# Kernel tuning notes

Measured on AMD Instinct MI355X. Metric: run time of the kernel, lower is better.

Reference implementation:

```python
import jax, jax.numpy as jnp
import numpy as np

NEG_POS_RATIO = 3
BETA = 1.0
ALPHA = 2.0


def _smooth_ex_loss(pred, tgt):
    # a = beta / (1 - exp(-alpha)); c = a - beta - beta/alpha
    a = BETA / (1.0 - np.exp(-ALPHA))
    c = a - BETA - BETA / ALPHA
    diff = jnp.abs(pred - tgt)
    return jnp.where(diff < 1.0,
                     a * (diff + (jnp.exp(-ALPHA * diff) - 1.0) / ALPHA),
                     BETA * diff + c)


def setup_inputs() -> dict:
    key = jax.random.key(0)
    k1, k2, k3, k4 = jax.random.split(key, 4)
    B, P, C = 128, 8732, 21
    return {
        "confidence": jax.random.normal(k1, (B, P, C), dtype=jnp.float32),
        "predicted_locations": jax.random.normal(k2, (B, P, 4), dtype=jnp.float32),
        "labels": jax.random.randint(k3, (B, P), 0, C, dtype=jnp.int64),
        "gt_locations": jax.random.normal(k4, (B, P, 4), dtype=jnp.float32),
    }


def reference(confidence, predicted_locations, labels, gt_locations):
    # confidence: [B, P, C]; labels: [B, P]; locations: [B, P, 4]
    logp = jax.nn.log_softmax(confidence, axis=2)
    pos_mask = labels > 0

    # --- hard negative mining (no-grad in original) ---
    bg_loss = jax.lax.stop_gradient(-logp[:, :, 0])          # [B, P]
    num_pos = pos_mask.sum(axis=1, keepdims=True)             # [B, 1]
    num_neg = num_pos * NEG_POS_RATIO
    mined = jnp.where(pos_mask, -jnp.inf, bg_loss)
    idx = jnp.argsort(-mined, axis=1)                         # descending sort
    orders = jnp.argsort(idx, axis=1)                         # rank of each prior
    neg_mask = orders < num_neg
    mask = pos_mask | neg_mask                                # [B, P]

    # --- classification loss: sum of CE over mined priors ---
    per_elem_ce = -jnp.take_along_axis(logp, labels[..., None], axis=2)[..., 0]
    classification_loss = jnp.sum(jnp.where(mask, per_elem_ce, 0.0))

    # --- localization loss: smooth-ex loss over positive priors ---
    loc = _smooth_ex_loss(predicted_locations, gt_locations)  # [B, P, 4]
    smooth_sum = jnp.sum(jnp.where(pos_mask[..., None], loc, 0.0))

    n_pos_total = pos_mask.sum().astype(jnp.float32)
    return (smooth_sum / n_pos_total, classification_loss / n_pos_total)
```

## Files before the change

kernel.cpp:

```cpp
#include <hip/hip_runtime.h>
#include <cstdint>


#define B_ 128
#define P_ 8732
#define C_ 21
constexpr int TPB = 256;
constexpr int TILE = 256;
constexpr int TPBATCH = 35;
constexpr int TAILCNT = P_ - (TPBATCH - 1) * TILE;
constexpr int NTILES = B_ * TPBATCH;
constexpr int TPBLK = 4;
constexpr int GRID = NTILES / TPBLK;
constexpr int TILE_F = TILE * C_;
constexpr int NCHUNK = TILE_F * 4 / 1024;

typedef const __attribute__((address_space(1))) uint32_t* gas_u32p;
typedef __attribute__((address_space(3))) uint32_t* las_u32p;

__device__ __forceinline__ float waveSumF(float v) {
#pragma unroll
  for (int o = 32; o; o >>= 1) v += __shfl_down(v, o);
  return v;
}
__device__ __forceinline__ int waveSumI(int v) {
#pragma unroll
  for (int o = 32; o; o >>= 1) v += __shfl_down(v, o);
  return v;
}
__device__ __forceinline__ double waveSumD(double v) {
#pragma unroll
  for (int o = 32; o; o >>= 1) v += __shfl_down(v, o);
  return v;
}

__device__ __forceinline__ void stage_tile(const float* __restrict__ src,
                                           float* dst, const char* clampEnd,
                                           int wid, int lane) {
  const char* base = (const char*)src;
  for (int j = wid; j < NCHUNK; j += 4) {
    const char* s = base + j * 1024 + lane * 16;
    if (s > clampEnd) s = clampEnd;
    __builtin_amdgcn_global_load_lds((gas_u32p)s, (las_u32p)(dst + j * 256), 16, 0, 0);
  }
}

__global__ __launch_bounds__(TPB) void k_main(
    const float* __restrict__ conf, const float* __restrict__ pred,
    const int* __restrict__ labels, const float* __restrict__ gt,
    float2* __restrict__ part, float* __restrict__ ceneg, int* __restrict__ npos) {
  __shared__ __align__(16) float tile[2][TILE_F];
  const int tid = threadIdx.x;
  const int wid = tid >> 6, lane = tid & 63;
  const int tau0 = blockIdx.x * TPBLK;
  const int b_first = tau0 / TPBATCH;
  const char* clampEnd = (const char*)conf + (size_t)B_ * P_ * C_ * 4 - 16;
  const float4* pred4 = (const float4*)pred;
  const float4* gt4 = (const float4*)gt;

  {
    const int b = tau0 / TPBATCH, x = tau0 - b * TPBATCH;
    stage_tile(conf + ((size_t)b * P_ + x * TILE) * C_, tile[0], clampEnd, wid, lane);
  }
  int lab_r;
  float4 pr_r, gt_r;
  {
    const int b = tau0 / TPBATCH, x = tau0 - b * TPBATCH;
    size_t gp = (size_t)b * P_ + (size_t)x * TILE + tid;
    if (gp > (size_t)B_ * P_ - 1) gp = (size_t)B_ * P_ - 1;
    lab_r = labels[gp];
    pr_r = pred4[gp];
    gt_r = gt4[gp];
  }
  __syncthreads();

  float sm_acc = 0.f, cp_acc = 0.f, cn0 = 0.f, cn1 = 0.f;
  int np0 = 0, np1 = 0;

#pragma unroll
  for (int k = 0; k < TPBLK; ++k) {
    const int tau = tau0 + k;
    const int cur = k & 1;

    int lab_n = 0;
    float4 pr_n = make_float4(0, 0, 0, 0), gt_n = pr_n;
    if (k + 1 < TPBLK) {
      const int tn = tau + 1;
      const int bn = tn / TPBATCH, xn = tn - bn * TPBATCH;
      stage_tile(conf + ((size_t)bn * P_ + xn * TILE) * C_, tile[cur ^ 1], clampEnd, wid, lane);
      size_t gp = (size_t)bn * P_ + (size_t)xn * TILE + tid;
      if (gp > (size_t)B_ * P_ - 1) gp = (size_t)B_ * P_ - 1;
      lab_n = labels[gp];
      pr_n = pred4[gp];
      gt_n = gt4[gp];
    }

    const int b = tau / TPBATCH, x = tau - b * TPBATCH;
    const int cnt = (x == TPBATCH - 1) ? TAILCNT : TILE;
    if (tid < cnt) {
      const float* row = &tile[cur][tid * C_];
      float m = row[0];
#pragma unroll
      for (int c = 1; c < C_; ++c) m = fmaxf(m, row[c]);
      float s = 0.f;
#pragma unroll
      for (int c = 0; c < C_; ++c) s += __expf(row[c] - m);
      const float lse = m + __logf(s);
      const float ce = lse - row[lab_r];
      float ce_neg = 0.f;
      int np = 0;
      if (lab_r > 0) {
        np = 1;
        cp_acc += ce;
        const float A = 1.1565176427496657f;
        const float Cc = -0.3434823572503343f;
        float d;
        d = fabsf(pr_r.x - gt_r.x); sm_acc += (d < 1.f) ? A * (d + (__expf(-2.f * d) - 1.f) * 0.5f) : d + Cc;
        d = fabsf(pr_r.y - gt_r.y); sm_acc += (d < 1.f) ? A * (d + (__expf(-2.f * d) - 1.f) * 0.5f) : d + Cc;
        d = fabsf(pr_r.z - gt_r.z); sm_acc += (d < 1.f) ? A * (d + (__expf(-2.f * d) - 1.f) * 0.5f) : d + Cc;
        d = fabsf(pr_r.w - gt_r.w); sm_acc += (d < 1.f) ? A * (d + (__expf(-2.f * d) - 1.f) * 0.5f) : d + Cc;
      } else {
        ce_neg = ce;
      }
      if (b == b_first) { cn0 += ce_neg; np0 += np; }
      else             { cn1 += ce_neg; np1 += np; }
    }

    __syncthreads();
    lab_r = lab_n; pr_r = pr_n; gt_r = gt_n;
  }

  float sm = waveSumF(sm_acc), cp = waveSumF(cp_acc);
  float c0 = waveSumF(cn0), c1 = waveSumF(cn1);
  int n0 = waveSumI(np0), n1 = waveSumI(np1);
  float* red = tile[0];
  int* redi = (int*)red;
  if (lane == 0) {
    red[wid] = sm; red[4 + wid] = cp; red[8 + wid] = c0; red[12 + wid] = c1;
    redi[16 + wid] = n0; redi[20 + wid] = n1;
  }
  __syncthreads();
  if (tid == 0) {
    float SM = 0, CP = 0, C0 = 0, C1 = 0;
    int N0 = 0, N1 = 0;
#pragma unroll
    for (int w = 0; w < 4; ++w) {
      SM += red[w]; CP += red[4 + w]; C0 += red[8 + w]; C1 += red[12 + w];
      N0 += redi[16 + w]; N1 += redi[20 + w];
    }
    part[blockIdx.x] = make_float2(SM, CP);
    atomicAdd(&ceneg[b_first], C0);
    atomicAdd(&npos[b_first], N0);
    const int b_last = (tau0 + TPBLK - 1) / TPBATCH;
    if (b_last != b_first) {
      atomicAdd(&ceneg[b_last], C1);
      atomicAdd(&npos[b_last], N1);
    }
  }
}

__global__ __launch_bounds__(TPB) void k_decide(double* __restrict__ g,
                                                const float2* __restrict__ part,
                                                const float* __restrict__ ceneg,
                                                const int* __restrict__ npos,
                                                int* __restrict__ flags) {
  const int tid = threadIdx.x;
  const int wid = tid >> 6, lane = tid & 63;
  __shared__ double sd0[4], sd1[4], sd2[4];
  __shared__ int si[4];

  double sm = 0.0, cp = 0.0;
  for (int i = tid; i < GRID; i += TPB) {
    const float2 v = part[i];
    sm += (double)v.x;
    cp += (double)v.y;
  }
  sm = waveSumD(sm);
  cp = waveSumD(cp);
  if (lane == 0) { sd0[wid] = sm; sd1[wid] = cp; }
  __syncthreads();
  if (tid == 0) {
    g[0] = sd0[0] + sd0[1] + sd0[2] + sd0[3];
    g[1] = sd1[0] + sd1[1] + sd1[2] + sd1[3];
  }
  __syncthreads();

  double cn = 0.0;
  int n = 0;
  if (tid < B_) {
    const int np = npos[tid];
    const int need = 3 * np;
    const int nav = P_ - np;
    int fl = 0;
    if (need >= nav) cn = (double)ceneg[tid]; else fl = 1;
    flags[tid] = fl;
    n = np;
  }
  cn = waveSumD(cn);
  n = waveSumI(n);
  if (lane == 0) { sd2[wid] = cn; si[wid] = n; }
  __syncthreads();
  if (tid == 0) {
    g[2] = sd2[0] + sd2[1] + sd2[2] + sd2[3];
    g[3] = (double)(si[0] + si[1] + si[2] + si[3]);
  }
}

__device__ __forceinline__ unsigned keyCE(const float* __restrict__ conf,
                                          const int* __restrict__ labels,
                                          int b, int p, float& ce) {
  const float* row = conf + ((size_t)b * P_ + p) * C_;
  float m = row[0];
  for (int c = 1; c < C_; ++c) m = fmaxf(m, row[c]);
  float s = 0.f;
  for (int c = 0; c < C_; ++c) s += __expf(row[c] - m);
  const float lse = m + __logf(s);
  const int lab = labels[(size_t)b * P_ + p];
  ce = lse - row[lab];
  if (lab > 0) return 0u;
  unsigned u = __float_as_uint(lse - row[0]);
  u = (u & 0x80000000u) ? ~u : (u | 0x80000000u);
  return u ? u : 1u;
}

__global__ __launch_bounds__(TPB) void k_fallback(const float* __restrict__ conf,
                                                  const int* __restrict__ labels,
                                                  double* __restrict__ g,
                                                  const int* __restrict__ npos,
                                                  const int* __restrict__ flags) {
  const int b = blockIdx.x;
  if (!flags[b]) return;
  const int tid = threadIdx.x;
  const int need = 3 * npos[b];
  __shared__ int icnt[4];
  __shared__ float fsum[4];

  unsigned long long lo = 1, hi = 0xFFFFFFFFull, ans = 1;
  while (lo <= hi) {
    const unsigned long long mid = lo + ((hi - lo) >> 1);
    int c = 0;
    float dummy;
    for (int p = tid; p < P_; p += TPB)
      if ((unsigned long long)keyCE(conf, labels, b, p, dummy) >= mid) c++;
    c = waveSumI(c);
    if ((tid & 63) == 0) icnt[tid >> 6] = c;
    __syncthreads();
    const int tot = icnt[0] + icnt[1] + icnt[2] + icnt[3];
    if (tot >= need) { ans = mid; lo = mid + 1; } else { hi = mid - 1; }
    __syncthreads();
  }

  int cgt = 0;
  float sgt = 0.f;
  for (int p = tid; p < P_; p += TPB) {
    float ce;
    const unsigned long long k = keyCE(conf, labels, b, p, ce);
    if (k > ans) { cgt++; sgt += ce; }
  }
  cgt = waveSumI(cgt);
  sgt = waveSumF(sgt);
  if ((tid & 63) == 0) { icnt[tid >> 6] = cgt; fsum[tid >> 6] = sgt; }
  __syncthreads();
  if (tid == 0) {
    const int gtot = icnt[0] + icnt[1] + icnt[2] + icnt[3];
    double s = (double)(fsum[0] + fsum[1] + fsum[2] + fsum[3]);
    int r = need - gtot;
    int taken = 0;
    for (int p = 0; p < P_ && taken < r; ++p) {
      float ce;
      if (keyCE(conf, labels, b, p, ce) == ans) { s += ce; taken++; }
    }
    atomicAdd(&g[2], s);
  }
}

__global__ void k_final(const double* __restrict__ g, float* __restrict__ out) {
  out[0] = (float)(g[0] / g[3]);
  out[1] = (float)((g[1] + g[2]) / g[3]);
}

extern "C" void kernel_launch(void* const* d_in, const int* in_sizes, int n_in,
                              void* d_out, int out_size, void* d_ws, size_t ws_size,
                              hipStream_t stream) {
  const float* conf = (const float*)d_in[0];
  const float* pred = (const float*)d_in[1];
  const int* labels = (const int*)d_in[2];
  const float* gt = (const float*)d_in[3];
  float* out = (float*)d_out;

  double* g = (double*)d_ws;
  float* ceneg = (float*)(g + 8);
  int* npos = (int*)(ceneg + B_);
  int* flags = npos + B_;
  float2* part = (float2*)(flags + B_);
  const size_t zbytes = 8 * sizeof(double) + B_ * sizeof(float) + B_ * sizeof(int);
  hipMemsetAsync(d_ws, 0, zbytes, stream);

  hipLaunchKernelGGL(k_main, dim3(GRID), dim3(TPB), 0, stream,
                     conf, pred, labels, gt, part, ceneg, npos);
  hipLaunchKernelGGL(k_decide, dim3(1), dim3(TPB), 0, stream, g, part, ceneg, npos, flags);
  hipLaunchKernelGGL(k_fallback, dim3(B_), dim3(TPB), 0, stream, conf, labels, g, npos, flags);
  hipLaunchKernelGGL(k_final, dim3(1), dim3(1), 0, stream, g, out);
}
```

Baseline: 39.13 us.

## Merge decide, fallback and final kernels into one tail kernel; halve block size

Replaces the three post-processing kernels (decide, fallback, final) with a single one-block tail kernel that reduces the partials, runs the per-batch fallback selection serially when needed, and writes the output directly. This removes two kernel launches and their launch gaps. Separately, the main kernel moves to 128-thread blocks with 128-prior tiles, so it launches twice as many blocks, and staging now skips out-of-range chunks instead of clamping the address. The fallback path is now serialized across batches in one block, which would be very slow if any batch ever needs it.

Result: slower. 48.26 us (+23.3%).

```diff
diff --git a/kernel.cpp b/kernel.cpp
--- a/kernel.cpp
+++ b/kernel.cpp
@@ -5,15 +5,15 @@
 #define B_ 128
 #define P_ 8732
 #define C_ 21
-constexpr int TPB = 256;
-constexpr int TILE = 256;
-constexpr int TPBATCH = 35;
-constexpr int TAILCNT = P_ - (TPBATCH - 1) * TILE;
-constexpr int NTILES = B_ * TPBATCH;
+constexpr int TPB = 128;
+constexpr int TILE = 128;
+constexpr int TPROW = 69;
+constexpr int TAILCNT = P_ - (TPROW - 1) * TILE;
+constexpr int NTILES = B_ * TPROW;
 constexpr int TPBLK = 4;
 constexpr int GRID = NTILES / TPBLK;
 constexpr int TILE_F = TILE * C_;
-constexpr int NCHUNK = TILE_F * 4 / 1024;
+constexpr int NCHUNK = 11;
 
 typedef const __attribute__((address_space(1))) uint32_t* gas_u32p;
 typedef __attribute__((address_space(3))) uint32_t* las_u32p;
@@ -35,13 +35,14 @@
 }
 
 __device__ __forceinline__ void stage_tile(const float* __restrict__ src,
-                                           float* dst, const char* clampEnd,
+                                           float* dst, int tilebytes,
                                            int wid, int lane) {
   const char* base = (const char*)src;
-  for (int j = wid; j < NCHUNK; j += 4) {
-    const char* s = base + j * 1024 + lane * 16;
-    if (s > clampEnd) s = clampEnd;
-    __builtin_amdgcn_global_load_lds((gas_u32p)s, (las_u32p)(dst + j * 256), 16, 0, 0);
+  for (int j = wid; j < NCHUNK; j += 2) {
+    const int off = (j << 10) + (lane << 4);
+    if (off < tilebytes)
+      __builtin_amdgcn_global_load_lds((gas_u32p)(base + off),
+                                       (las_u32p)(dst + (j << 8)), 16, 0, 0);
   }
 }
 
@@ -53,19 +54,19 @@
   const int tid = threadIdx.x;
   const int wid = tid >> 6, lane = tid & 63;
   const int tau0 = blockIdx.x * TPBLK;
-  const int b_first = tau0 / TPBATCH;
-  const char* clampEnd = (const char*)conf + (size_t)B_ * P_ * C_ * 4 - 16;
+  const int b_first = tau0 / TPROW;
   const float4* pred4 = (const float4*)pred;
   const float4* gt4 = (const float4*)gt;
 
   {
-    const int b = tau0 / TPBATCH, x = tau0 - b * TPBATCH;
-    stage_tile(conf + ((size_t)b * P_ + x * TILE) * C_, tile[0], clampEnd, wid, lane);
+    const int b = tau0 / TPROW, x = tau0 - b * TPROW;
+    const int tb = ((x == TPROW - 1) ? TAILCNT : TILE) * (C_ * 4);
+    stage_tile(conf + ((size_t)b * P_ + (size_t)x * TILE) * C_, tile[0], tb, wid, lane);
   }
   int lab_r;
   float4 pr_r, gt_r;
   {
-    const int b = tau0 / TPBATCH, x = tau0 - b * TPBATCH;
+    const int b = tau0 / TPROW, x = tau0 - b * TPROW;
     size_t gp = (size_t)b * P_ + (size_t)x * TILE + tid;
     if (gp > (size_t)B_ * P_ - 1) gp = (size_t)B_ * P_ - 1;
     lab_r = labels[gp];
@@ -86,8 +87,9 @@
     float4 pr_n = make_float4(0, 0, 0, 0), gt_n = pr_n;
     if (k + 1 < TPBLK) {
       const int tn = tau + 1;
-      const int bn = tn / TPBATCH, xn = tn - bn * TPBATCH;
-      stage_tile(conf + ((size_t)bn * P_ + xn * TILE) * C_, tile[cur ^ 1], clampEnd, wid, lane);
+      const int bn = tn / TPROW, xn = tn - bn * TPROW;
+      const int tb = ((xn == TPROW - 1) ? TAILCNT : TILE) * (C_ * 4);
+      stage_tile(conf + ((size_t)bn * P_ + (size_t)xn * TILE) * C_, tile[cur ^ 1], tb, wid, lane);
       size_t gp = (size_t)bn * P_ + (size_t)xn * TILE + tid;
       if (gp > (size_t)B_ * P_ - 1) gp = (size_t)B_ * P_ - 1;
       lab_n = labels[gp];
@@ -95,8 +97,8 @@
       gt_n = gt4[gp];
     }
 
-    const int b = tau / TPBATCH, x = tau - b * TPBATCH;
-    const int cnt = (x == TPBATCH - 1) ? TAILCNT : TILE;
+    const int b = tau / TPROW, x = tau - b * TPROW;
+    const int cnt = (x == TPROW - 1) ? TAILCNT : TILE;
     if (tid < cnt) {
       const float* row = &tile[cur][tid * C_];
       float m = row[0];
@@ -136,73 +138,22 @@
   float* red = tile[0];
   int* redi = (int*)red;
   if (lane == 0) {
-    red[wid] = sm; red[4 + wid] = cp; red[8 + wid] = c0; red[12 + wid] = c1;
-    redi[16 + wid] = n0; redi[20 + wid] = n1;
+    red[wid] = sm; red[2 + wid] = cp; red[4 + wid] = c0; red[6 + wid] = c1;
+    redi[8 + wid] = n0; redi[10 + wid] = n1;
   }
   __syncthreads();
   if (tid == 0) {
-    float SM = 0, CP = 0, C0 = 0, C1 = 0;
-    int N0 = 0, N1 = 0;
-#pragma unroll
-    for (int w = 0; w < 4; ++w) {
-      SM += red[w]; CP += red[4 + w]; C0 += red[8 + w]; C1 += red[12 + w];
-      N0 += redi[16 + w]; N1 += redi[20 + w];
-    }
+    float SM = red[0] + red[1], CP = red[2] + red[3];
+    float C0 = red[4] + red[5], C1 = red[6] + red[7];
+    int N0 = redi[8] + redi[9], N1 = redi[10] + redi[11];
     part[blockIdx.x] = make_float2(SM, CP);
     atomicAdd(&ceneg[b_first], C0);
     atomicAdd(&npos[b_first], N0);
-    const int b_last = (tau0 + TPBLK - 1) / TPBATCH;
+    const int b_last = (tau0 + TPBLK - 1) / TPROW;
     if (b_last != b_first) {
       atomicAdd(&ceneg[b_last], C1);
       atomicAdd(&npos[b_last], N1);
     }
-  }
-}
-
-__global__ __launch_bounds__(TPB) void k_decide(double* __restrict__ g,
-                                                const float2* __restrict__ part,
-                                                const float* __restrict__ ceneg,
-                                                const int* __restrict__ npos,
-                                                int* __restrict__ flags) {
-  const int tid = threadIdx.x;
-  const int wid = tid >> 6, lane = tid & 63;
-  __shared__ double sd0[4], sd1[4], sd2[4];
-  __shared__ int si[4];
-
-  double sm = 0.0, cp = 0.0;
-  for (int i = tid; i < GRID; i += TPB) {
-    const float2 v = part[i];
-    sm += (double)v.x;
-    cp += (double)v.y;
-  }
-  sm = waveSumD(sm);
-  cp = waveSumD(cp);
-  if (lane == 0) { sd0[wid] = sm; sd1[wid] = cp; }
-  __syncthreads();
-  if (tid == 0) {
-    g[0] = sd0[0] + sd0[1] + sd0[2] + sd0[3];
-    g[1] = sd1[0] + sd1[1] + sd1[2] + sd1[3];
-  }
-  __syncthreads();
-
-  double cn = 0.0;
-  int n = 0;
-  if (tid < B_) {
-    const int np = npos[tid];
-    const int need = 3 * np;
-    const int nav = P_ - np;
-    int fl = 0;
-    if (need >= nav) cn = (double)ceneg[tid]; else fl = 1;
-    flags[tid] = fl;
-    n = np;
-  }
-  cn = waveSumD(cn);
-  n = waveSumI(n);
-  if (lane == 0) { sd2[wid] = cn; si[wid] = n; }
-  __syncthreads();
-  if (tid == 0) {
-    g[2] = sd2[0] + sd2[1] + sd2[2] + sd2[3];
-    g[3] = (double)(si[0] + si[1] + si[2] + si[3]);
   }
 }
 
@@ -223,60 +174,94 @@
   return u ? u : 1u;
 }
 
-__global__ __launch_bounds__(TPB) void k_fallback(const float* __restrict__ conf,
-                                                  const int* __restrict__ labels,
-                                                  double* __restrict__ g,
-                                                  const int* __restrict__ npos,
-                                                  const int* __restrict__ flags) {
-  const int b = blockIdx.x;
-  if (!flags[b]) return;
+__global__ __launch_bounds__(256) void k_tail(
+    const float2* __restrict__ part, const float* __restrict__ ceneg,
+    const int* __restrict__ npos, const float* __restrict__ conf,
+    const int* __restrict__ labels, float* __restrict__ out) {
   const int tid = threadIdx.x;
-  const int need = 3 * npos[b];
+  const int wid = tid >> 6, lane = tid & 63;
+  __shared__ double sd0[4], sd1[4], sd2[4];
+  __shared__ int si[4];
+  __shared__ int s_flag[B_];
+  __shared__ double s_extra;
   __shared__ int icnt[4];
   __shared__ float fsum[4];
 
-  unsigned long long lo = 1, hi = 0xFFFFFFFFull, ans = 1;
-  while (lo <= hi) {
-    const unsigned long long mid = lo + ((hi - lo) >> 1);
-    int c = 0;
-    float dummy;
-    for (int p = tid; p < P_; p += TPB)
-      if ((unsigned long long)keyCE(conf, labels, b, p, dummy) >= mid) c++;
-    c = waveSumI(c);
-    if ((tid & 63) == 0) icnt[tid >> 6] = c;
+  double sm = 0.0, cp = 0.0;
+  for (int i = tid; i < GRID; i += 256) {
+    const float2 v = part[i];
+    sm += (double)v.x;
+    cp += (double)v.y;
+  }
+  sm = waveSumD(sm);
+  cp = waveSumD(cp);
+  if (lane == 0) { sd0[wid] = sm; sd1[wid] = cp; }
+
+  double cn = 0.0;
+  int n = 0;
+  if (tid < B_) {
+    const int np = npos[tid];
+    const int fl = (3 * np < P_ - np) ? 1 : 0;
+    s_flag[tid] = fl;
+    if (!fl) cn = (double)ceneg[tid];
+    n = np;
+  }
+  cn = waveSumD(cn);
+  n = waveSumI(n);
+  if (lane == 0) { sd2[wid] = cn; si[wid] = n; }
+  if (tid == 0) s_extra = 0.0;
+  __syncthreads();
+
+  for (int b = 0; b < B_; ++b) {
+    if (!s_flag[b]) continue;
+    const int need = 3 * npos[b];
+    unsigned long long lo = 1, hi = 0xFFFFFFFFull, ans = 1;
+    while (lo <= hi) {
+      const unsigned long long mid = lo + ((hi - lo) >> 1);
+      int c = 0;
+      float dummy;
+      for (int p = tid; p < P_; p += 256)
+        if ((unsigned long long)keyCE(conf, labels, b, p, dummy) >= mid) c++;
+      c = waveSumI(c);
+      if (lane == 0) icnt[wid] = c;
+      __syncthreads();
+      const int tot = icnt[0] + icnt[1] + icnt[2] + icnt[3];
+      if (tot >= need) { ans = mid; lo = mid + 1; } else { hi = mid - 1; }
+      __syncthreads();
+    }
+    int cgt = 0;
+    float sgt = 0.f;
+    for (int p = tid; p < P_; p += 256) {
+      float ce;
+      const unsigned long long k = keyCE(conf, labels, b, p, ce);
+      if (k > ans) { cgt++; sgt += ce; }
+    }
+    cgt = waveSumI(cgt);
+    sgt = waveSumF(sgt);
+    if (lane == 0) { icnt[wid] = cgt; fsum[wid] = sgt; }
     __syncthreads();
-    const int tot = icnt[0] + icnt[1] + icnt[2] + icnt[3];
-    if (tot >= need) { ans = mid; lo = mid + 1; } else { hi = mid - 1; }
+    if (tid == 0) {
+      const int gtot = icnt[0] + icnt[1] + icnt[2] + icnt[3];
+      double s = (double)(fsum[0] + fsum[1] + fsum[2] + fsum[3]);
+      int r = need - gtot;
+      int taken = 0;
+      for (int p = 0; p < P_ && taken < r; ++p) {
+        float ce;
+        if (keyCE(conf, labels, b, p, ce) == ans) { s += ce; taken++; }
+      }
+      s_extra += s;
+    }
     __syncthreads();
   }
 
-  int cgt = 0;
-  float sgt = 0.f;
-  for (int p = tid; p < P_; p += TPB) {
-    float ce;
-    const unsigned long long k = keyCE(conf, labels, b, p, ce);
-    if (k > ans) { cgt++; sgt += ce; }
-  }
-  cgt = waveSumI(cgt);
-  sgt = waveSumF(sgt);
-  if ((tid & 63) == 0) { icnt[tid >> 6] = cgt; fsum[tid >> 6] = sgt; }
-  __syncthreads();
   if (tid == 0) {
-    const int gtot = icnt[0] + icnt[1] + icnt[2] + icnt[3];
-    double s = (double)(fsum[0] + fsum[1] + fsum[2] + fsum[3]);
-    int r = need - gtot;
-    int taken = 0;
-    for (int p = 0; p < P_ && taken < r; ++p) {
-      float ce;
-      if (keyCE(conf, labels, b, p, ce) == ans) { s += ce; taken++; }
-    }
-    atomicAdd(&g[2], s);
-  }
-}
-
-__global__ void k_final(const double* __restrict__ g, float* __restrict__ out) {
-  out[0] = (float)(g[0] / g[3]);
-  out[1] = (float)((g[1] + g[2]) / g[3]);
+    const double G0 = sd0[0] + sd0[1] + sd0[2] + sd0[3];
+    const double G1 = sd1[0] + sd1[1] + sd1[2] + sd1[3];
+    const double G2 = sd2[0] + sd2[1] + sd2[2] + sd2[3] + s_extra;
+    const double N = (double)(si[0] + si[1] + si[2] + si[3]);
+    out[0] = (float)(G0 / N);
+    out[1] = (float)((G1 + G2) / N);
+  }
 }
 
 extern "C" void kernel_launch(void* const* d_in, const int* in_sizes, int n_in,
@@ -288,17 +273,13 @@
   const float* gt = (const float*)d_in[3];
   float* out = (float*)d_out;
 
-  double* g = (double*)d_ws;
-  float* ceneg = (float*)(g + 8);
+  float* ceneg = (float*)d_ws;
   int* npos = (int*)(ceneg + B_);
-  int* flags = npos + B_;
-  float2* part = (float2*)(flags + B_);
-  const size_t zbytes = 8 * sizeof(double) + B_ * sizeof(float) + B_ * sizeof(int);
-  hipMemsetAsync(d_ws, 0, zbytes, stream);
+  float2* part = (float2*)(npos + B_);
+  hipMemsetAsync(d_ws, 0, B_ * (sizeof(float) + sizeof(int)), stream);
 
   hipLaunchKernelGGL(k_main, dim3(GRID), dim3(TPB), 0, stream,
                      conf, pred, labels, gt, part, ceneg, npos);
-  hipLaunchKernelGGL(k_decide, dim3(1), dim3(TPB), 0, stream, g, part, ceneg, npos, flags);
-  hipLaunchKernelGGL(k_fallback, dim3(B_), dim3(TPB), 0, stream, conf, labels, g, npos, flags);
-  hipLaunchKernelGGL(k_final, dim3(1), dim3(1), 0, stream, g, out);
-}
+  hipLaunchKernelGGL(k_tail, dim3(1), dim3(256), 0, stream,
+                     part, ceneg, npos, conf, labels, out);
+}
```
